# Kernel optimization log

Measured on AMD Instinct MI355X. Metric: run time of the kernel, lower is better.

## Reference

```python
import jax, jax.numpy as jnp
import numpy as np

E, H, I, K, T = 32, 2048, 768, 4, 2048


def setup_inputs() -> dict:
    key = jax.random.key(0)
    k1, k2, k3, k4, k5 = jax.random.split(key, 5)
    hidden_states = jax.random.normal(k1, (T, H), dtype=jnp.float32)
    top_k_index = jax.random.randint(k2, (T, K), 0, E, dtype=jnp.int64)
    top_k_weights = jax.random.uniform(k3, (T, K), dtype=jnp.float32)
    gate_up_proj = jax.random.normal(k4, (E, H, 2 * I), dtype=jnp.float32) * 0.02
    down_proj = jax.random.normal(k5, (E, I, H), dtype=jnp.float32) * 0.02
    return {
        "hidden_states": hidden_states,
        "top_k_index": top_k_index,
        "top_k_weights": top_k_weights,
        "gate_up_proj": gate_up_proj,
        "down_proj": down_proj,
    }


def reference(hidden_states, top_k_index, top_k_weights, gate_up_proj, down_proj):
    # Dense routing-weight matrix [T, E]: zeros scattered with top-k weights
    num_tokens = hidden_states.shape[0]
    routing = jnp.zeros((num_tokens, E), dtype=hidden_states.dtype)
    routing = routing.at[jnp.arange(num_tokens)[:, None], top_k_index].set(top_k_weights)

    # Batched (grouped) GEMM over all experts; weights are stored transposed
    # gate_up_proj: [E, H, 2I] -> gu: [E, T, 2I]
    gu = jnp.einsum('th,ehi->eti', hidden_states, gate_up_proj)
    gate, up = jnp.split(gu, 2, axis=-1)           # each [E, T, I]
    inter = jax.nn.silu(gate) * up                 # [E, T, I]
    # down_proj: [E, I, H] -> per-expert output [E, T, H]
    expert_out = jnp.einsum('eti,eih->eth', inter, down_proj)
    # Weighted combine over experts
    out = jnp.einsum('te,eth->th', routing, expert_out)
    return out
```

## Files before the change

### kernel.cpp

```cpp
#include <hip/hip_runtime.h>
#include <hip/hip_bf16.h>

#define E_ 32
#define H_ 2048
#define I_ 768
#define T_ 2048
#define TWO_I 1536
#define MAX_TILES 96

typedef __attribute__((ext_vector_type(8))) short short8;
typedef __attribute__((ext_vector_type(4))) float floatx4;

#define WS_OFFSETS 0
#define WS_IDS     1024
#define WS_WTS     (1024 + 32768)
#define WS_TILES   (1024 + 65536)
#define WS_SLOTTJ  69632
#define WS_INTER   131072
#define WS_HID16   (131072 + 8192*768*2)
#define WS_EO      21102592ULL

__device__ __forceinline__ unsigned short f2bf(float f) {
  union { float f; unsigned u; } v; v.f = f;
  unsigned r = v.u + 0x7FFFu + ((v.u >> 16) & 1u);
  return (unsigned short)(r >> 16);
}

__device__ __forceinline__ unsigned pkbf(float a, float b) {
  __hip_bfloat162 h = __float22bfloat162_rn(float2{a, b});
  union { __hip_bfloat162 h; unsigned u; } v; v.h = h; return v.u;
}

__device__ __forceinline__ void gload_lds16(const unsigned short* g, unsigned short* l) {
  __builtin_amdgcn_global_load_lds(
      (__attribute__((address_space(1))) void*)g,
      (__attribute__((address_space(3))) void*)l, 16, 0, 0);
}

__global__ void build_routing(const int* __restrict__ idx, const float* __restrict__ w,
                              char* __restrict__ ws) {
  int* offs = (int*)(ws + WS_OFFSETS);
  int* ids  = (int*)(ws + WS_IDS);
  float* wt = (float*)(ws + WS_WTS);
  int* tiles = (int*)(ws + WS_TILES);
  int* slot_tj = (int*)(ws + WS_SLOTTJ);
  __shared__ int s_cnt[E_];
  __shared__ int s_pos[E_];
  int tid = threadIdx.x;
  if (tid < E_) s_cnt[tid] = 0;
  __syncthreads();
  for (int i = tid; i < T_ * 4; i += 256) {
    int t = i >> 2, j = i & 3;
    int e = idx[i];
    bool keep = true;
    for (int j2 = j + 1; j2 < 4; ++j2) if (idx[t * 4 + j2] == e) keep = false;
    if (keep) atomicAdd(&s_cnt[e], 1);
  }
  __syncthreads();
  if (tid == 0) {
    int run = 0;
    for (int e = 0; e < E_; ++e) { offs[e] = run; s_pos[e] = run; run += s_cnt[e]; }
    offs[E_] = run;
    int nt = 0;
    for (int e = 0; e < E_; ++e)
      for (int m0 = 0; m0 < s_cnt[e]; m0 += 128) tiles[nt++] = (e << 16) | (m0 >> 7);
    for (; nt < MAX_TILES; ++nt) tiles[nt] = -1;
  }
  __syncthreads();
  for (int i = tid; i < T_ * 4; i += 256) {
    int t = i >> 2, j = i & 3;
    int e = idx[i];
    bool keep = true;
    for (int j2 = j + 1; j2 < 4; ++j2) if (idx[t * 4 + j2] == e) keep = false;
    if (keep) {
      int p = atomicAdd(&s_pos[e], 1);
      ids[p] = t;
      wt[p] = w[i];
      slot_tj[i] = p;
    } else {
      slot_tj[i] = -1;
    }
  }
}

__global__ void cvt_hidden(const float* __restrict__ hs, char* __restrict__ ws) {
  int g = blockIdx.x * 256 + threadIdx.x;
  const float4 f0 = ((const float4*)hs)[g * 2];
  const float4 f1 = ((const float4*)hs)[g * 2 + 1];
  uint4 o;
  o.x = pkbf(f0.x, f0.y); o.y = pkbf(f0.z, f0.w);
  o.z = pkbf(f1.x, f1.y); o.w = pkbf(f1.z, f1.w);
  ((uint4*)(ws + WS_HID16))[g] = o;
}

__global__ __launch_bounds__(256, 2) void gemm1(
    const float* __restrict__ gup, char* __restrict__ ws) {
  const int* offs = (const int*)(ws + WS_OFFSETS);
  const int* ids  = (const int*)(ws + WS_IDS);
  const int* tiles = (const int*)(ws + WS_TILES);
  const unsigned short* h16 = (const unsigned short*)(ws + WS_HID16);
  unsigned short* inter = (unsigned short*)(ws + WS_INTER);

  int tl = tiles[blockIdx.y];
  if (tl < 0) return;
  int e = tl >> 16, m0 = (tl & 0xffff) << 7;
  int start = offs[e];
  int mrem = offs[e + 1] - start - m0;
  int n0 = blockIdx.x * 64;

  __shared__ __align__(16) unsigned short Al[2][128 * 64];
  __shared__ __align__(16) unsigned short Bl[2][128][72];

  int tid = threadIdx.x, lane = tid & 63, wid = tid >> 6;
  int wy = wid >> 1, wx = wid & 1, quad = lane >> 4, l15 = lane & 15;

  floatx4 acc[4][4] = {};

  const unsigned short* aSrc[4];
#pragma unroll
  for (int u = 0; u < 4; ++u) {
    int s = (wid * 4 + u) * 64 + lane;
    int r = s >> 3;
    int c = (s & 7) ^ (r & 7);
    int tok = ids[start + m0 + ((r < mrem) ? r : 0)];
    aSrc[u] = h16 + (size_t)tok * H_ + c * 8;
  }
  const float* gB[4];
  int brow0[4], bofs[4];
#pragma unroll
  for (int pp = 0; pp < 4; ++pp) {
    int lin2 = tid + 256 * pp;
    int k2 = lin2 >> 5, c4 = lin2 & 31;
    int gcol = (c4 < 16) ? (n0 + c4 * 4) : (I_ + n0 + (c4 - 16) * 4);
    gB[pp] = gup + (size_t)e * H_ * TWO_I + (size_t)(2 * k2) * TWO_I + gcol;
    brow0[pp] = c4 * 4;
    bofs[pp] = (((k2 >> 2) ^ (c4 & 7)) * 8) + (k2 & 3) * 2;
  }

  float4 pf0[4], pf1[4];

  auto loadB = [&](int kb) {
#pragma unroll
    for (int pp = 0; pp < 4; ++pp) {
      const float* p = gB[pp] + (size_t)kb * 64 * TWO_I;
      pf0[pp] = *(const float4*)p;
      pf1[pp] = *(const float4*)(p + TWO_I);
    }
  };
  auto stageA = [&](int kb, int buf) {
#pragma unroll
    for (int u = 0; u < 4; ++u)
      gload_lds16(aSrc[u] + kb * 64, &Al[buf][(wid * 4 + u) * 512]);
  };
  auto writeB = [&](int buf) {
#pragma unroll
    for (int pp = 0; pp < 4; ++pp) {
      *(unsigned*)&Bl[buf][brow0[pp] + 0][bofs[pp]] = pkbf(pf0[pp].x, pf1[pp].x);
      *(unsigned*)&Bl[buf][brow0[pp] + 1][bofs[pp]] = pkbf(pf0[pp].y, pf1[pp].y);
      *(unsigned*)&Bl[buf][brow0[pp] + 2][bofs[pp]] = pkbf(pf0[pp].z, pf1[pp].z);
      *(unsigned*)&Bl[buf][brow0[pp] + 3][bofs[pp]] = pkbf(pf0[pp].w, pf1[pp].w);
    }
  };
  auto compute = [&](int buf) {
#pragma unroll
    for (int ks = 0; ks < 2; ++ks) {
      short8 af[4], bfr[4];
#pragma unroll
      for (int mi = 0; mi < 4; ++mi) {
        int row = wy * 64 + mi * 16 + l15;
        int c16 = (ks * 4 + quad) ^ (row & 7);
        af[mi] = *(const short8*)&Al[buf][row * 64 + c16 * 8];
      }
#pragma unroll
      for (int ni = 0; ni < 4; ++ni) {
        int j = (ni < 2) ? (wx * 32 + ni * 16 + l15) : (64 + wx * 32 + (ni - 2) * 16 + l15);
        int ch = (ks * 4 + quad) ^ ((j >> 2) & 7);
        bfr[ni] = *(const short8*)&Bl[buf][j][ch * 8];
      }
#pragma unroll
      for (int mi = 0; mi < 4; ++mi)
#pragma unroll
        for (int ni = 0; ni < 4; ++ni)
          acc[mi][ni] = __builtin_amdgcn_mfma_f32_16x16x32_bf16(af[mi], bfr[ni], acc[mi][ni], 0, 0, 0);
    }
  };

  const int NK = H_ / 64;
  loadB(0);
  stageA(0, 0);
  writeB(0);
  __syncthreads();

  for (int kb = 0; kb < NK; ++kb) {
    int cur = kb & 1, nxt = cur ^ 1;
    if (kb + 1 < NK) {
      loadB(kb + 1);
      stageA(kb + 1, nxt);
    }
    compute(cur);
    __builtin_amdgcn_sched_barrier(0);
    if (kb + 1 < NK) writeB(nxt);
    __syncthreads();
  }

#pragma unroll
  for (int mi = 0; mi < 4; ++mi) {
#pragma unroll
    for (int r = 0; r < 4; ++r) {
      int row = wy * 64 + mi * 16 + quad * 4 + r;
      if (row < mrem) {
        int slot = start + m0 + row;
#pragma unroll
        for (int ni = 0; ni < 2; ++ni) {
          float g = acc[mi][ni][r];
          float u = acc[mi][ni + 2][r];
          float s = g / (1.f + __expf(-g));
          int col = n0 + wx * 32 + ni * 16 + l15;
          inter[(size_t)slot * I_ + col] = f2bf(s * u);
        }
      }
    }
  }
}

__global__ __launch_bounds__(256, 2) void gemm2(
    const float* __restrict__ down, char* __restrict__ ws) {
  const int* offs = (const int*)(ws + WS_OFFSETS);
  const int* ids  = (const int*)(ws + WS_IDS);
  const float* wt = (const float*)(ws + WS_WTS);
  const int* tiles = (const int*)(ws + WS_TILES);
  const unsigned short* inter = (const unsigned short*)(ws + WS_INTER);
  float* eo = (float*)(ws + WS_EO);

  int tl = tiles[blockIdx.y];
  if (tl < 0) return;
  int e = tl >> 16, m0 = (tl & 0xffff) << 7;
  int start = offs[e];
  int mrem = offs[e + 1] - start - m0;
  int n0 = blockIdx.x * 128;

  __shared__ __align__(16) unsigned short Al[2][128 * 64];
  __shared__ __align__(16) unsigned short Bl[2][128][72];

  int tid = threadIdx.x, lane = tid & 63, wid = tid >> 6;
  int wy = wid >> 1, wx = wid & 1, quad = lane >> 4, l15 = lane & 15;

  floatx4 acc[4][4] = {};

  const unsigned short* aSrc[4];
#pragma unroll
  for (int u = 0; u < 4; ++u) {
    int s = (wid * 4 + u) * 64 + lane;
    int r = s >> 3;
    int c = (s & 7) ^ (r & 7);
    int arow = (r < mrem) ? r : 0;
    aSrc[u] = inter + (size_t)(start + m0 + arow) * I_ + c * 8;
  }
  const float* gB[4];
  int brow0[4], bofs[4];
#pragma unroll
  for (int pp = 0; pp < 4; ++pp) {
    int lin2 = tid + 256 * pp;
    int k2 = lin2 >> 5, c4 = lin2 & 31;
    gB[pp] = down + (size_t)e * I_ * H_ + (size_t)(2 * k2) * H_ + (n0 + c4 * 4);
    brow0[pp] = c4 * 4;
    bofs[pp] = (((k2 >> 2) ^ (c4 & 7)) * 8) + (k2 & 3) * 2;
  }

  float4 pf0[4], pf1[4];

  auto loadB = [&](int kb) {
#pragma unroll
    for (int pp = 0; pp < 4; ++pp) {
      const float* p = gB[pp] + (size_t)kb * 64 * H_;
      pf0[pp] = *(const float4*)p;
      pf1[pp] = *(const float4*)(p + H_);
    }
  };
  auto stageA = [&](int kb, int buf) {
#pragma unroll
    for (int u = 0; u < 4; ++u)
      gload_lds16(aSrc[u] + kb * 64, &Al[buf][(wid * 4 + u) * 512]);
  };
  auto writeB = [&](int buf) {
#pragma unroll
    for (int pp = 0; pp < 4; ++pp) {
      *(unsigned*)&Bl[buf][brow0[pp] + 0][bofs[pp]] = pkbf(pf0[pp].x, pf1[pp].x);
      *(unsigned*)&Bl[buf][brow0[pp] + 1][bofs[pp]] = pkbf(pf0[pp].y, pf1[pp].y);
      *(unsigned*)&Bl[buf][brow0[pp] + 2][bofs[pp]] = pkbf(pf0[pp].z, pf1[pp].z);
      *(unsigned*)&Bl[buf][brow0[pp] + 3][bofs[pp]] = pkbf(pf0[pp].w, pf1[pp].w);
    }
  };
  auto compute = [&](int buf) {
#pragma unroll
    for (int ks = 0; ks < 2; ++ks) {
      short8 af[4], bfr[4];
#pragma unroll
      for (int mi = 0; mi < 4; ++mi) {
        int row = wy * 64 + mi * 16 + l15;
        int c16 = (ks * 4 + quad) ^ (row & 7);
        af[mi] = *(const short8*)&Al[buf][row * 64 + c16 * 8];
      }
#pragma unroll
      for (int ni = 0; ni < 4; ++ni) {
        int j = wx * 64 + ni * 16 + l15;
        int ch = (ks * 4 + quad) ^ ((j >> 2) & 7);
        bfr[ni] = *(const short8*)&Bl[buf][j][ch * 8];
      }
#pragma unroll
      for (int mi = 0; mi < 4; ++mi)
#pragma unroll
        for (int ni = 0; ni < 4; ++ni)
          acc[mi][ni] = __builtin_amdgcn_mfma_f32_16x16x32_bf16(af[mi], bfr[ni], acc[mi][ni], 0, 0, 0);
    }
  };

  const int NK = I_ / 64;
  loadB(0);
  stageA(0, 0);
  writeB(0);
  __syncthreads();

  for (int kb = 0; kb < NK; ++kb) {
    int cur = kb & 1, nxt = cur ^ 1;
    if (kb + 1 < NK) {
      loadB(kb + 1);
      stageA(kb + 1, nxt);
    }
    compute(cur);
    __builtin_amdgcn_sched_barrier(0);
    if (kb + 1 < NK) writeB(nxt);
    __syncthreads();
  }

#pragma unroll
  for (int mi = 0; mi < 4; ++mi) {
#pragma unroll
    for (int r = 0; r < 4; ++r) {
      int row = wy * 64 + mi * 16 + quad * 4 + r;
      if (row < mrem) {
        int slot = start + m0 + row;
        float wv = wt[slot];
#pragma unroll
        for (int ni = 0; ni < 4; ++ni) {
          int col = n0 + wx * 64 + ni * 16 + l15;
          eo[(size_t)slot * H_ + col] = wv * acc[mi][ni][r];
        }
      }
    }
  }
}

__global__ void combine(float* __restrict__ out, const char* __restrict__ ws) {
  const int* slot_tj = (const int*)(ws + WS_SLOTTJ);
  const float* eo = (const float*)(ws + WS_EO);
  int g = blockIdx.x * 256 + threadIdx.x;
  int token = g >> 9, c4 = g & 511;
  const int* st = slot_tj + token * 4;
  float4 s = {0.f, 0.f, 0.f, 0.f};
#pragma unroll
  for (int j = 0; j < 4; ++j) {
    int p = st[j];
    if (p >= 0) {
      const float4 v = *(const float4*)(eo + (size_t)p * H_ + c4 * 4);
      s.x += v.x; s.y += v.y; s.z += v.z; s.w += v.w;
    }
  }
  *(float4*)(out + (size_t)token * H_ + c4 * 4) = s;
}

extern "C" void kernel_launch(void* const* d_in, const int* in_sizes, int n_in,
                              void* d_out, int out_size, void* d_ws, size_t ws_size,
                              hipStream_t stream) {
  (void)in_sizes; (void)n_in; (void)out_size; (void)ws_size;
  const float* hidden = (const float*)d_in[0];
  const int* idx      = (const int*)d_in[1];
  const float* w      = (const float*)d_in[2];
  const float* gup    = (const float*)d_in[3];
  const float* down   = (const float*)d_in[4];
  float* out = (float*)d_out;
  char* ws = (char*)d_ws;

  build_routing<<<1, 256, 0, stream>>>(idx, w, ws);
  cvt_hidden<<<T_ * H_ / 8 / 256, 256, 0, stream>>>(hidden, ws);
  gemm1<<<dim3(I_ / 64, MAX_TILES), 256, 0, stream>>>(gup, ws);
  gemm2<<<dim3(H_ / 128, MAX_TILES), 256, 0, stream>>>(down, ws);
  combine<<<T_ * H_ / 4 / 256, 256, 0, stream>>>(out, ws);
}
```

Baseline: 831.6 us.

## Replace syncthreads with partial vmcnt waits and explicit barriers in MoE GEMM loops

Both grouped-GEMM main loops now use hand-placed s_waitcnt with a partial vmcnt count and raw s_barrier instead of __syncthreads. The intent is to keep the next tile's global B loads in flight while the current tile computes, instead of draining all memory counters at each barrier. The last iteration is peeled so the loop body carries no conditionals. The hardcoded vmcnt(12) assumes a specific number of outstanding loads per stage. If that count is wrong, the code could read stale data or stall.

Result: no change. 819.1 us (-1.5%).

```diff
diff --git a/kernel.cpp b/kernel.cpp
--- a/kernel.cpp
+++ b/kernel.cpp
@@ -189,18 +189,32 @@
   loadB(0);
   stageA(0, 0);
   writeB(0);
-  __syncthreads();
-
-  for (int kb = 0; kb < NK; ++kb) {
+  asm volatile("s_waitcnt vmcnt(0) lgkmcnt(0)" ::: "memory");
+  __builtin_amdgcn_sched_barrier(0);
+  __builtin_amdgcn_s_barrier();
+  __builtin_amdgcn_sched_barrier(0);
+
+  for (int kb = 0; kb < NK - 1; ++kb) {
     int cur = kb & 1, nxt = cur ^ 1;
-    if (kb + 1 < NK) {
-      loadB(kb + 1);
-      stageA(kb + 1, nxt);
-    }
+    loadB(kb + 1);
+    stageA(kb + 1, nxt);
+    asm volatile("s_waitcnt vmcnt(12) lgkmcnt(0)" ::: "memory");
+    __builtin_amdgcn_sched_barrier(0);
+    __builtin_amdgcn_s_barrier();
+    __builtin_amdgcn_sched_barrier(0);
     compute(cur);
     __builtin_amdgcn_sched_barrier(0);
-    if (kb + 1 < NK) writeB(nxt);
-    __syncthreads();
+    __builtin_amdgcn_s_barrier();
+    __builtin_amdgcn_sched_barrier(0);
+    writeB(nxt);
+  }
+  {
+    int cur = (NK - 1) & 1;
+    asm volatile("s_waitcnt vmcnt(0) lgkmcnt(0)" ::: "memory");
+    __builtin_amdgcn_sched_barrier(0);
+    __builtin_amdgcn_s_barrier();
+    __builtin_amdgcn_sched_barrier(0);
+    compute(cur);
   }
 
 #pragma unroll
@@ -319,18 +333,32 @@
   loadB(0);
   stageA(0, 0);
   writeB(0);
-  __syncthreads();
-
-  for (int kb = 0; kb < NK; ++kb) {
+  asm volatile("s_waitcnt vmcnt(0) lgkmcnt(0)" ::: "memory");
+  __builtin_amdgcn_sched_barrier(0);
+  __builtin_amdgcn_s_barrier();
+  __builtin_amdgcn_sched_barrier(0);
+
+  for (int kb = 0; kb < NK - 1; ++kb) {
     int cur = kb & 1, nxt = cur ^ 1;
-    if (kb + 1 < NK) {
-      loadB(kb + 1);
-      stageA(kb + 1, nxt);
-    }
+    loadB(kb + 1);
+    stageA(kb + 1, nxt);
+    asm volatile("s_waitcnt vmcnt(12) lgkmcnt(0)" ::: "memory");
+    __builtin_amdgcn_sched_barrier(0);
+    __builtin_amdgcn_s_barrier();
+    __builtin_amdgcn_sched_barrier(0);
     compute(cur);
     __builtin_amdgcn_sched_barrier(0);
-    if (kb + 1 < NK) writeB(nxt);
-    __syncthreads();
+    __builtin_amdgcn_s_barrier();
+    __builtin_amdgcn_sched_barrier(0);
+    writeB(nxt);
+  }
+  {
+    int cur = (NK - 1) & 1;
+    asm volatile("s_waitcnt vmcnt(0) lgkmcnt(0)" ::: "memory");
+    __builtin_amdgcn_sched_barrier(0);
+    __builtin_amdgcn_s_barrier();
+    __builtin_amdgcn_sched_barrier(0);
+    compute(cur);
   }
 
 #pragma unroll
```
